# Performance work log

Hardware: AMD Instinct MI355X
Metric: run time of the kernel (lower is better)

Reference implementation:

```python
import jax, jax.numpy as jnp
import numpy as np

N_HEAD = 16
D_MODEL = 1024
D_HEAD = D_MODEL // N_HEAD
B, T = 2, 2048


def setup_inputs() -> dict:
    key = jax.random.key(0)
    k1, k2, k3 = jax.random.split(key, 3)
    x = jax.random.normal(k1, (B, T, D_MODEL), dtype=jnp.float32)
    w_attn = jax.random.normal(k2, (3 * D_MODEL, D_MODEL), dtype=jnp.float32) * (D_MODEL ** -0.5)
    w_proj = jax.random.normal(k3, (D_MODEL, D_MODEL), dtype=jnp.float32) * (D_MODEL ** -0.5)
    return {"x": x, "w_attn": w_attn, "w_proj": w_proj}


def _rms_norm(x):
    eps = jnp.asarray(jnp.finfo(x.dtype).eps, x.dtype)
    var = jnp.mean(jnp.square(x), axis=-1, keepdims=True)
    return x * jax.lax.rsqrt(var + eps)


def _rotate_half(x):
    x1, x2 = jnp.split(x, 2, axis=-1)
    return jnp.concatenate((-x2, x1), axis=-1)


def reference(x, w_attn, w_proj):
    Bx, Tx, C = x.shape
    qkv = jnp.einsum('btc,fc->btf', x, w_attn)  # [B,T,3C]
    q, k, v = jnp.split(qkv, 3, axis=-1)
    # [B, H, T, Dh]
    q = q.reshape(Bx, Tx, N_HEAD, D_HEAD).transpose(0, 2, 1, 3)
    k = k.reshape(Bx, Tx, N_HEAD, D_HEAD).transpose(0, 2, 1, 3)
    v = v.reshape(Bx, Tx, N_HEAD, D_HEAD).transpose(0, 2, 1, 3)
    # QK RMSNorm (no learned weight)
    q = _rms_norm(q)
    k = _rms_norm(k)
    # Rotary embedding over full d_head: freqs tiled twice
    inv_freq = 1.0 / (10000.0 ** (jnp.arange(0, D_HEAD, 2, dtype=jnp.float32) / D_HEAD))
    t = jnp.arange(Tx, dtype=jnp.float32)
    freqs = jnp.einsum('i,j->ij', t, inv_freq)  # [T, Dh/2]
    emb = jnp.concatenate((freqs, freqs), axis=-1)  # [T, Dh]
    cos = jnp.cos(emb)[None, None, :, :]
    sin = jnp.sin(emb)[None, None, :, :]
    q = q * cos + _rotate_half(q) * sin
    k = k * cos + _rotate_half(k) * sin
    # Causal SDPA
    scale = D_HEAD ** -0.5
    scores = jnp.einsum('bhqd,bhkd->bhqk', q, k) * scale
    causal = jnp.tril(jnp.ones((Tx, Tx), dtype=bool))
    scores = jnp.where(causal[None, None], scores, jnp.asarray(-jnp.inf, scores.dtype))
    attn = jax.nn.softmax(scores, axis=-1)
    y = jnp.einsum('bhqk,bhkd->bhqd', attn, v)
    y = y.transpose(0, 2, 1, 3).reshape(Bx, Tx, C)
    return jnp.einsum('btc,oc->bto', y, w_proj)
```

## Files before the change

kernel.cpp:

```cpp
#include <hip/hip_runtime.h>
#include <cstdint>
#include <cstddef>


typedef short bf16x8 __attribute__((ext_vector_type(8)));
typedef float floatx4 __attribute__((ext_vector_type(4)));
typedef float floatx2 __attribute__((ext_vector_type(2)));
typedef unsigned short ushortx8 __attribute__((ext_vector_type(8)));
typedef unsigned short ushortx4 __attribute__((ext_vector_type(4)));
typedef unsigned int uintx2 __attribute__((ext_vector_type(2)));

#define DEVI __device__ __forceinline__

DEVI float bf2f(unsigned short u) {
    unsigned int x = ((unsigned int)u) << 16;
    return __builtin_bit_cast(float, x);
}
DEVI unsigned short f2bf(float f) {
    unsigned int u = __builtin_bit_cast(unsigned int, f);
    u += 0x7fffu + ((u >> 16) & 1u);
    return (unsigned short)(u >> 16);
}
DEVI unsigned int pkbf2(float a, float b) {
    unsigned int ua = __builtin_bit_cast(unsigned int, a) + 0x8000u;
    unsigned int ub = __builtin_bit_cast(unsigned int, b) + 0x8000u;
    return __builtin_amdgcn_perm(ub, ua, 0x07060302);
}

DEVI void glds16(const unsigned short* g, unsigned short* l) {
    __builtin_amdgcn_global_load_lds(
        (const __attribute__((address_space(1))) unsigned int*)g,
        (__attribute__((address_space(3))) unsigned int*)l, 16, 0, 0);
}

DEVI void cast8(unsigned short* dst, const float* src) {
    floatx4 a = *(const floatx4*)src;
    floatx4 b = *(const floatx4*)(src + 4);
    ushortx8 o;
    o[0] = f2bf(a[0]); o[1] = f2bf(a[1]); o[2] = f2bf(a[2]); o[3] = f2bf(a[3]);
    o[4] = f2bf(b[0]); o[5] = f2bf(b[1]); o[6] = f2bf(b[2]); o[7] = f2bf(b[3]);
    *(ushortx8*)dst = o;
}

__global__ __launch_bounds__(256)
void cast_inputs(const float* __restrict__ x, const float* __restrict__ wa,
                 const float* __restrict__ wp,
                 unsigned short* __restrict__ xb, unsigned short* __restrict__ wab,
                 unsigned short* __restrict__ wpb, float* __restrict__ ropetab)
{
    size_t g = (size_t)blockIdx.x * 256 + threadIdx.x;
    size_t stride = (size_t)gridDim.x * 256;
    for (size_t i = g; i < (4194304 / 8); i += stride) cast8(xb  + i * 8, x  + i * 8);
    for (size_t i = g; i < (3145728 / 8); i += stride) cast8(wab + i * 8, wa + i * 8);
    for (size_t i = g; i < (1048576 / 8); i += stride) cast8(wpb + i * 8, wp + i * 8);
    for (size_t i = g; i < 65536; i += stride) {
        int t = (int)(i >> 5), f = (int)(i & 31);
        float ang = (float)t * __expf(-(float)f * 0.28782313662425572f);
        float sn, cs;
        __sincosf(ang, &sn, &cs);
        ropetab[2 * i]     = cs;
        ropetab[2 * i + 1] = sn;
    }
}

__global__ __launch_bounds__(512, 2)
void gemm_qkv_8ph(const unsigned short* __restrict__ A,
                  const unsigned short* __restrict__ B,
                  const float* __restrict__ ropetab,
                  unsigned short* __restrict__ Cqk,
                  unsigned short* __restrict__ Vt)
{
    __shared__ __align__(16) unsigned short lds[2][2][256 * 64];

    const int tid  = threadIdx.x;
    const int lane = tid & 63;
    const int w    = tid >> 6;
    const int wm   = w >> 2;
    const int wn   = w & 3;
    const int quad = lane >> 4;
    const int lm   = lane & 15;

    const int lin = blockIdx.y * 12 + blockIdx.x;
    const int s   = (lin & 7) * 24 + (lin >> 3);
    const int m0  = (s / 12) * 256;
    const int n0  = (s % 12) * 256;

    const int srow = tid >> 3;
    const int scol = (((tid & 7) ^ ((tid >> 3) & 7)) * 8);
    const int ldst = w * 512;

#define STG_A(u, WBi, kq) glds16(&A[(size_t)(m0 + (u) * 64 + srow) * 1024 + (kq) + scol], \
                                 &lds[WBi][0][(u) * 4096 + ldst])
#define STG_B(u, WBi, kq) glds16(&B[(size_t)(n0 + (u) * 64 + srow) * 1024 + (kq) + scol], \
                                 &lds[WBi][1][(u) * 4096 + ldst])
#define RD_A(RBi, rrow, kk) (*(const bf16x8*)&lds[RBi][0][(rrow) * 64 + ((((kk) * 4 + quad) ^ ((rrow) & 7)) * 8)])
#define RD_B(RBi, rrow, kk) (*(const bf16x8*)&lds[RBi][1][(rrow) * 64 + ((((kk) * 4 + quad) ^ ((rrow) & 7)) * 8)])

    floatx4 acc[8][4] = {};
    bf16x8 afr[4][2];
    bf16x8 bfr[4][2];

#define MQ(MB, JB)                                                              \
  do {                                                                          \
    _Pragma("unroll")                                                           \
    for (int kk = 0; kk < 2; ++kk)                                              \
      _Pragma("unroll")                                                         \
      for (int mi = 0; mi < 4; ++mi)                                            \
        _Pragma("unroll")                                                       \
        for (int j2 = 0; j2 < 2; ++j2)                                          \
          acc[(MB) + mi][(JB) + j2] = __builtin_amdgcn_mfma_f32_16x16x32_bf16(  \
              afr[mi][kk], bfr[(JB) + j2][kk], acc[(MB) + mi][(JB) + j2], 0, 0, 0); \
  } while (0)

#define TILE(RBi, WBi, KT, LASTF)                                               \
  do {                                                                          \
    const int kn = ((KT) + 1) * 64;                                             \
                \
    if (!(LASTF)) { STG_B(0, WBi, kn); STG_B(1, WBi, kn); }                     \
    _Pragma("unroll")                                                           \
    for (int kk = 0; kk < 2; ++kk) {                                            \
      _Pragma("unroll")                                                         \
      for (int mi = 0; mi < 4; ++mi)                                            \
        afr[mi][kk] = RD_A(RBi, wm * 128 + mi * 16 + lm, kk);                   \
      _Pragma("unroll")                                                         \
      for (int j2 = 0; j2 < 2; ++j2)                                            \
        bfr[j2][kk] = RD_B(RBi, wn * 64 + j2 * 16 + lm, kk);                    \
    }                                                                           \
    asm volatile("s_waitcnt lgkmcnt(8)" ::: "memory");                          \
    __builtin_amdgcn_s_barrier();                                               \
    asm volatile("s_waitcnt lgkmcnt(0)" ::: "memory");                          \
    __builtin_amdgcn_s_setprio(1); MQ(0, 0); __builtin_amdgcn_s_setprio(0);     \
    __builtin_amdgcn_s_barrier();                                               \
               \
    if (!(LASTF)) { STG_B(2, WBi, kn); STG_B(3, WBi, kn); }                     \
    _Pragma("unroll")                                                           \
    for (int kk = 0; kk < 2; ++kk)                                              \
      _Pragma("unroll")                                                         \
      for (int j2 = 0; j2 < 2; ++j2)                                            \
        bfr[2 + j2][kk] = RD_B(RBi, wn * 64 + (2 + j2) * 16 + lm, kk);          \
    if (!(LASTF)) { asm volatile("s_waitcnt vmcnt(4)" ::: "memory"); }          \
    else          { asm volatile("s_waitcnt vmcnt(0)" ::: "memory"); }          \
    __builtin_amdgcn_s_barrier();                                               \
    asm volatile("s_waitcnt lgkmcnt(0)" ::: "memory");                          \
    __builtin_amdgcn_s_setprio(1); MQ(0, 2); __builtin_amdgcn_s_setprio(0);     \
    __builtin_amdgcn_s_barrier();                                               \
                           \
    if (!(LASTF)) { STG_A(0, WBi, kn); STG_A(2, WBi, kn); }                     \
    _Pragma("unroll")                                                           \
    for (int kk = 0; kk < 2; ++kk)                                              \
      _Pragma("unroll")                                                         \
      for (int mi = 0; mi < 4; ++mi)                                            \
        afr[mi][kk] = RD_A(RBi, wm * 128 + 64 + mi * 16 + lm, kk);              \
    __builtin_amdgcn_s_barrier();                                               \
    asm volatile("s_waitcnt lgkmcnt(0)" ::: "memory");                          \
    __builtin_amdgcn_s_setprio(1); MQ(4, 2); __builtin_amdgcn_s_setprio(0);     \
    __builtin_amdgcn_s_barrier();                                               \
      \
    if (!(LASTF)) { STG_A(1, WBi, kn); STG_A(3, WBi, kn);                       \
                    asm volatile("s_waitcnt vmcnt(2)" ::: "memory"); }          \
    __builtin_amdgcn_s_barrier();                                               \
    __builtin_amdgcn_s_setprio(1); MQ(4, 0); __builtin_amdgcn_s_setprio(0);     \
    __builtin_amdgcn_s_barrier();                                               \
  } while (0)

    STG_B(0, 0, 0); STG_B(1, 0, 0); STG_B(2, 0, 0); STG_B(3, 0, 0);
    STG_A(0, 0, 0); STG_A(2, 0, 0); STG_A(1, 0, 0); STG_A(3, 0, 0);
    asm volatile("s_waitcnt vmcnt(2)" ::: "memory");
    __builtin_amdgcn_s_barrier();

    for (int kt = 0; kt < 14; kt += 2) {
        TILE(0, 1, kt, false);
        TILE(1, 0, kt + 1, false);
    }
    TILE(0, 1, 14, false);
    TILE(1, 0, 15, true);

    const bool is_v = (n0 + wn * 64) >= 2048;
    if (!is_v) {
        const floatx2* rtab = (const floatx2*)ropetab;
        #pragma unroll
        for (int mi = 0; mi < 8; ++mi) {
            float rn[4];
            #pragma unroll
            for (int r = 0; r < 4; ++r) {
                float ss = 0.0f;
                #pragma unroll
                for (int j = 0; j < 4; ++j) ss += acc[mi][j][r] * acc[mi][j][r];
                ss += __shfl_xor(ss, 1, 64);
                ss += __shfl_xor(ss, 2, 64);
                ss += __shfl_xor(ss, 4, 64);
                ss += __shfl_xor(ss, 8, 64);
                rn[r] = rsqrtf(ss * (1.0f / 64.0f) + 1.1920929e-07f);
            }
            #pragma unroll
            for (int r = 0; r < 4; ++r) {
                int row = m0 + wm * 128 + mi * 16 + quad * 4 + r;
                int t = row & 2047;
                floatx2 cs0 = rtab[t * 32 + lm];
                floatx2 cs1 = rtab[t * 32 + 16 + lm];
                float g = rn[r];
                #pragma unroll
                for (int j = 0; j < 4; ++j) {
                    int d = j * 16 + lm;
                    float cs = (j & 1) ? cs1[0] : cs0[0];
                    float sn = (j & 1) ? cs1[1] : cs0[1];
                    float v  = acc[mi][j][r] * g;
                    float vp = acc[mi][j ^ 2][r] * g;
                    float sgn = (d < 32) ? -1.0f : 1.0f;
                    Cqk[(size_t)row * 2048 + (n0 + wn * 64 + d)] =
                        f2bf(v * cs + sgn * vp * sn);
                }
            }
        }
    } else {
        #pragma unroll
        for (int mi = 0; mi < 8; ++mi)
            #pragma unroll
            for (int j = 0; j < 4; ++j) {
                int col  = n0 + wn * 64 + j * 16 + lm;
                int row0 = m0 + wm * 128 + mi * 16 + quad * 4;
                int bq = row0 >> 11, t0 = row0 & 2047;
                ushortx4 pk;
                #pragma unroll
                for (int r = 0; r < 4; ++r) pk[r] = f2bf(acc[mi][j][r]);
                *(ushortx4*)&Vt[((size_t)(bq * 1024 + (col - 2048))) * 2048 + t0] = pk;
            }
    }
#undef TILE
#undef MQ
#undef RD_A
#undef RD_B
#undef STG_A
#undef STG_B
}

template <bool QKV_SPLIT, int BN, int BK>
__global__ __launch_bounds__(256)
void gemm_bt(const unsigned short* __restrict__ A, const unsigned short* __restrict__ B,
             unsigned short* __restrict__ Cqk, float* __restrict__ Cf,
             unsigned short* __restrict__ Vt, int M, int N, int K)
{
    constexpr int WCOLS = (BN == 128) ? 2 : 1;
    constexpr int WROWS = 4 / WCOLS;
    constexpr int MI    = 128 / (16 * WROWS);
    constexpr int LPR   = BK / 8;
    constexpr int RPI   = 64 / LPR;

    __shared__ __align__(16) unsigned short As[128 * BK];
    __shared__ __align__(16) unsigned short Bs[BN * BK];

    const int tid  = threadIdx.x;
    const int lane = tid & 63;
    const int w    = tid >> 6;
    const int wm   = w / WCOLS, wn = w % WCOLS;
    const int quad = lane >> 4;
    const int lm   = lane & 15;
    const int m0 = blockIdx.y * 128;
    const int n0 = blockIdx.x * BN;
    const int sr = lane / LPR;
    const int sc = (lane % LPR) * 8;

    floatx4 acc[MI][4] = {};

    for (int k0 = 0; k0 < K; k0 += BK) {
        __syncthreads();
        #pragma unroll
        for (int i = 0; i < 32 / RPI; ++i) {
            int r = w * 32 + i * RPI;
            glds16(&A[(size_t)(m0 + r + sr) * K + k0 + sc], &As[r * BK]);
        }
        #pragma unroll
        for (int i = 0; i < (BN / 4) / RPI; ++i) {
            int r = w * (BN / 4) + i * RPI;
            glds16(&B[(size_t)(n0 + r + sr) * K + k0 + sc], &Bs[r * BK]);
        }
        __syncthreads();

        #pragma unroll
        for (int kk = 0; kk < BK / 32; ++kk) {
            bf16x8 a[MI];
            #pragma unroll
            for (int i = 0; i < MI; ++i)
                a[i] = *(const bf16x8*)&As[(wm * (16 * MI) + i * 16 + lm) * BK + kk * 32 + quad * 8];
            #pragma unroll
            for (int j = 0; j < 4; ++j) {
                bf16x8 b = *(const bf16x8*)&Bs[(wn * 64 + j * 16 + lm) * BK + kk * 32 + quad * 8];
                #pragma unroll
                for (int i = 0; i < MI; ++i)
                    acc[i][j] = __builtin_amdgcn_mfma_f32_16x16x32_bf16(a[i], b, acc[i][j], 0, 0, 0);
            }
        }
    }

    if constexpr (QKV_SPLIT) {
    } else {
        #pragma unroll
        for (int i = 0; i < MI; ++i)
            #pragma unroll
            for (int j = 0; j < 4; ++j) {
                int col  = n0 + wn * 64 + j * 16 + lm;
                int row0 = m0 + wm * (16 * MI) + i * 16 + quad * 4;
                #pragma unroll
                for (int r = 0; r < 4; ++r)
                    Cf[(size_t)(row0 + r) * N + col] = acc[i][j][r];
            }
    }
}

#define ATTN_STEP(KSc, VSc, KSn, VSn, KT, DG, LAST)                            \
  do {                                                                         \
    if (!(LAST)) {                                                             \
      *(ushortx8*)&(KSn)[r0 * LD + pc] = kreg0;                                \
      *(ushortx8*)&(KSn)[r1 * LD + pc] = kreg1;                                \
      *(ushortx8*)&(VSn)[r0 * LD + pc] = vreg0;                                \
      *(ushortx8*)&(VSn)[r1 * LD + pc] = vreg1;                                \
      if ((KT) + 2 <= qt) {                                                    \
        kreg0 = *(const ushortx8*)kp0; kreg1 = *(const ushortx8*)kp1;          \
        vreg0 = *(const ushortx8*)vp0; vreg1 = *(const ushortx8*)vp1;          \
        kp0 += (size_t)64 * 2048; kp1 += (size_t)64 * 2048;                    \
        vp0 += 64; vp1 += 64;                                                  \
      }                                                                        \
    }                                                                          \
    floatx4 sa[4] = {};                                                        \
    _Pragma("unroll")                                                          \
    for (int kk = 0; kk < 2; ++kk)                                             \
      _Pragma("unroll")                                                        \
      for (int j = 0; j < 4; ++j) {                                            \
        bf16x8 kf = *(const bf16x8*)&(KSc)[(j * 16 + lm) * LD + kk * 32 + quad * 8]; \
        sa[j] = __builtin_amdgcn_mfma_f32_16x16x32_bf16(kf, qf[kk], sa[j], 0, 0, 0); \
      }                                                                        \
    _Pragma("unroll")                                                          \
    for (int j = 0; j < 4; ++j) {                                              \
      float p0 = exp2f(sa[j][0] * c1 - c2);                                    \
      float p1 = exp2f(sa[j][1] * c1 - c2);                                    \
      float p2 = exp2f(sa[j][2] * c1 - c2);                                    \
      float p3 = exp2f(sa[j][3] * c1 - c2);                                    \
      if (DG) {                                                                \
        int kb = (KT) * 64 + j * 16 + quad * 4;                                \
        if (kb + 0 > qrow) p0 = 0.0f;                                          \
        if (kb + 1 > qrow) p1 = 0.0f;                                          \
        if (kb + 2 > qrow) p2 = 0.0f;                                          \
        if (kb + 3 > qrow) p3 = 0.0f;                                          \
      }                                                                        \
      uintx2 pk;                                                               \
      pk[0] = pkbf2(p0, p1);                                                   \
      pk[1] = pkbf2(p2, p3);                                                   \
      *(uintx2*)&QPs[(w * 16 + lm) * LD + j * 16 + quad * 4] = pk;             \
    }                                                                          \
    _Pragma("unroll")                                                          \
    for (int kk = 0; kk < 2; ++kk) {                                           \
      bf16x8 pf = *(const bf16x8*)&QPs[(w * 16 + lm) * LD + kk * 32 + quad * 8]; \
      _Pragma("unroll")                                                        \
      for (int j = 0; j < 4; ++j) {                                            \
        bf16x8 vf = *(const bf16x8*)&(VSc)[(j * 16 + lm) * LD + kk * 32 + quad * 8]; \
        o[j] = __builtin_amdgcn_mfma_f32_16x16x32_bf16(pf, vf, o[j], 0, 0, 0); \
      }                                                                        \
      l_acc = __builtin_amdgcn_mfma_f32_16x16x32_bf16(pf, ones, l_acc, 0, 0, 0); \
    }                                                                          \
    if (!(LAST)) __syncthreads();                                              \
  } while (0)

__global__ __launch_bounds__(256)
void attention(const unsigned short* __restrict__ qk,
               const unsigned short* __restrict__ Vt,
               unsigned short* __restrict__ Y)
{
    constexpr int LD = 72;
    __shared__ __align__(16) unsigned short QPs[64 * LD];
    __shared__ __align__(16) unsigned short Ks0[64 * LD];
    __shared__ __align__(16) unsigned short Ks1[64 * LD];
    __shared__ __align__(16) unsigned short Vs0[64 * LD];
    __shared__ __align__(16) unsigned short Vs1[64 * LD];

    const int tid  = threadIdx.x;
    const int lane = tid & 63;
    const int w    = tid >> 6;
    const int quad = lane >> 4;
    const int lm   = lane & 15;

    const int bh = blockIdx.x;
    const int qt = 31 - blockIdx.y;
    const int b  = bh >> 4, h = bh & 15;
    const int q0 = qt * 64;
    const int qrow = q0 + w * 16 + lm;

    const int r0 = tid >> 3, r1 = r0 + 32, pc = (tid & 7) * 8;
    const unsigned short* kp0 = qk + (size_t)b * 2048 * 2048 + 1024 + h * 64
                              + (size_t)r0 * 2048 + pc;
    const unsigned short* kp1 = kp0 + (size_t)32 * 2048;
    const unsigned short* vp0 = Vt + (size_t)bh * 64 * 2048 + (size_t)r0 * 2048 + pc;
    const unsigned short* vp1 = vp0 + (size_t)32 * 2048;

    #pragma unroll
    for (int i = 0; i < 2; ++i) {
        int c = i * 256 + tid, row = c >> 3, col = (c & 7) * 8;
        *(ushortx8*)&QPs[row * LD + col] =
            *(const ushortx8*)&qk[((size_t)(b * 2048 + q0 + row)) * 2048 + h * 64 + col];
    }

    ushortx8 kreg0 = *(const ushortx8*)kp0, kreg1 = *(const ushortx8*)kp1;
    ushortx8 vreg0 = *(const ushortx8*)vp0, vreg1 = *(const ushortx8*)vp1;
    kp0 += (size_t)64 * 2048; kp1 += (size_t)64 * 2048;
    vp0 += 64; vp1 += 64;
    *(ushortx8*)&Ks0[r0 * LD + pc] = kreg0;
    *(ushortx8*)&Ks0[r1 * LD + pc] = kreg1;
    *(ushortx8*)&Vs0[r0 * LD + pc] = vreg0;
    *(ushortx8*)&Vs0[r1 * LD + pc] = vreg1;
    if (qt >= 1) {
        kreg0 = *(const ushortx8*)kp0; kreg1 = *(const ushortx8*)kp1;
        vreg0 = *(const ushortx8*)vp0; vreg1 = *(const ushortx8*)vp1;
        kp0 += (size_t)64 * 2048; kp1 += (size_t)64 * 2048;
        vp0 += 64; vp1 += 64;
    }
    __syncthreads();

    bf16x8 qf[2];
    #pragma unroll
    for (int kk = 0; kk < 2; ++kk)
        qf[kk] = *(const bf16x8*)&QPs[(w * 16 + lm) * LD + kk * 32 + quad * 8];

    bf16x8 ones;
    #pragma unroll
    for (int i = 0; i < 8; ++i) ones[i] = (short)0x3F80;

    floatx4 o[4] = {};
    floatx4 l_acc = {};
    const float c1 = 0.125f * 1.44269504f;
    const float c2 = 8.0f   * 1.44269504f;

    int kt = 0;
    for (; kt + 1 < qt; kt += 2) {
        ATTN_STEP(Ks0, Vs0, Ks1, Vs1, kt,     false, false);
        ATTN_STEP(Ks1, Vs1, Ks0, Vs0, kt + 1, false, false);
    }
    if (kt < qt) {
        ATTN_STEP(Ks0, Vs0, Ks1, Vs1, kt, false, false);
        ATTN_STEP(Ks1, Vs1, Ks0, Vs0, qt, true, true);
    } else {
        ATTN_STEP(Ks0, Vs0, Ks1, Vs1, qt, true, true);
    }

    float rinv[4];
    #pragma unroll
    for (int r = 0; r < 4; ++r) rinv[r] = 1.0f / l_acc[r];

    #pragma unroll
    for (int j = 0; j < 4; ++j) {
        int colg = h * 64 + j * 16 + lm;
        #pragma unroll
        for (int r = 0; r < 4; ++r) {
            int rowg = q0 + w * 16 + quad * 4 + r;
            Y[((size_t)(b * 2048 + rowg)) * 1024 + colg] = f2bf(o[j][r] * rinv[r]);
        }
    }
}

extern "C" void kernel_launch(void* const* d_in, const int* in_sizes, int n_in,
                              void* d_out, int out_size, void* d_ws, size_t ws_size,
                              hipStream_t stream)
{
    const float* x      = (const float*)d_in[0];
    const float* w_attn = (const float*)d_in[1];
    const float* w_proj = (const float*)d_in[2];
    float* out = (float*)d_out;

    unsigned short* qkbuf = (unsigned short*)d_ws;
    unsigned short* Vtb   = qkbuf + (size_t)4096 * 2048;
    unsigned short* y     = Vtb   + (size_t)32 * 64 * 2048;
    unsigned short* wpb   = y     + (size_t)4096 * 1024;
    unsigned short* xb  = (unsigned short*)d_out;
    unsigned short* wab = xb + (size_t)4096 * 1024;
    float* ropetab = (float*)(wab + (size_t)3072 * 1024);

    dim3 blk(256);
    cast_inputs<<<dim3(1024), blk, 0, stream>>>(x, w_attn, w_proj, xb, wab, wpb, ropetab);
    gemm_qkv_8ph<<<dim3(12, 16), dim3(512), 0, stream>>>(xb, wab, ropetab, qkbuf, Vtb);
    attention<<<dim3(32, 32), blk, 0, stream>>>(qkbuf, Vtb, y);
    gemm_bt<false, 64, 64>
        <<<dim3(16, 32), blk, 0, stream>>>(y, wpb, nullptr, out, nullptr, 4096, 1024, 1024);
}
```

Measured before the change: 176.2 us.

## Use 128-row query tiles with 512-thread attention blocks sharing K/V tiles

The attention kernel now processes 128 query rows per block with 8 waves (512 threads) instead of 64 rows with 4 waves. Each K/V tile loaded into shared memory is reused by twice as many query rows, which halves global K/V traffic and the number of blocks. Each thread now stages one 16-byte chunk of K and V instead of two. The last two key tiles are treated as diagonal, with causal masking, to cover the 128-row block. The gemm_bt template also drops an unused QKV-split path, which is cleanup. The trade-off is more wasted masked work on diagonal tiles, fewer blocks for load balance, and larger shared-memory use per block.

New measurement: 178.7 us. No clear change (+1.4%).

```diff
diff --git a/kernel.cpp b/kernel.cpp
--- a/kernel.cpp
+++ b/kernel.cpp
@@ -115,7 +115,6 @@
 #define TILE(RBi, WBi, KT, LASTF)                                               \
   do {                                                                          \
     const int kn = ((KT) + 1) * 64;                                             \
-                \
     if (!(LASTF)) { STG_B(0, WBi, kn); STG_B(1, WBi, kn); }                     \
     _Pragma("unroll")                                                           \
     for (int kk = 0; kk < 2; ++kk) {                                            \
@@ -131,7 +130,6 @@
     asm volatile("s_waitcnt lgkmcnt(0)" ::: "memory");                          \
     __builtin_amdgcn_s_setprio(1); MQ(0, 0); __builtin_amdgcn_s_setprio(0);     \
     __builtin_amdgcn_s_barrier();                                               \
-               \
     if (!(LASTF)) { STG_B(2, WBi, kn); STG_B(3, WBi, kn); }                     \
     _Pragma("unroll")                                                           \
     for (int kk = 0; kk < 2; ++kk)                                              \
@@ -144,7 +142,6 @@
     asm volatile("s_waitcnt lgkmcnt(0)" ::: "memory");                          \
     __builtin_amdgcn_s_setprio(1); MQ(0, 2); __builtin_amdgcn_s_setprio(0);     \
     __builtin_amdgcn_s_barrier();                                               \
-                           \
     if (!(LASTF)) { STG_A(0, WBi, kn); STG_A(2, WBi, kn); }                     \
     _Pragma("unroll")                                                           \
     for (int kk = 0; kk < 2; ++kk)                                              \
@@ -155,7 +152,6 @@
     asm volatile("s_waitcnt lgkmcnt(0)" ::: "memory");                          \
     __builtin_amdgcn_s_setprio(1); MQ(4, 2); __builtin_amdgcn_s_setprio(0);     \
     __builtin_amdgcn_s_barrier();                                               \
-      \
     if (!(LASTF)) { STG_A(1, WBi, kn); STG_A(3, WBi, kn);                       \
                     asm volatile("s_waitcnt vmcnt(2)" ::: "memory"); }          \
     __builtin_amdgcn_s_barrier();                                               \
@@ -234,11 +230,10 @@
 #undef STG_B
 }
 
-template <bool QKV_SPLIT, int BN, int BK>
+template <int BN, int BK>
 __global__ __launch_bounds__(256)
 void gemm_bt(const unsigned short* __restrict__ A, const unsigned short* __restrict__ B,
-             unsigned short* __restrict__ Cqk, float* __restrict__ Cf,
-             unsigned short* __restrict__ Vt, int M, int N, int K)
+             float* __restrict__ Cf, int M, int N, int K)
 {
     constexpr int WCOLS = (BN == 128) ? 2 : 1;
     constexpr int WROWS = 4 / WCOLS;
@@ -292,33 +287,26 @@
         }
     }
 
-    if constexpr (QKV_SPLIT) {
-    } else {
-        #pragma unroll
-        for (int i = 0; i < MI; ++i)
-            #pragma unroll
-            for (int j = 0; j < 4; ++j) {
-                int col  = n0 + wn * 64 + j * 16 + lm;
-                int row0 = m0 + wm * (16 * MI) + i * 16 + quad * 4;
-                #pragma unroll
-                for (int r = 0; r < 4; ++r)
-                    Cf[(size_t)(row0 + r) * N + col] = acc[i][j][r];
-            }
-    }
+    #pragma unroll
+    for (int i = 0; i < MI; ++i)
+        #pragma unroll
+        for (int j = 0; j < 4; ++j) {
+            int col  = n0 + wn * 64 + j * 16 + lm;
+            int row0 = m0 + wm * (16 * MI) + i * 16 + quad * 4;
+            #pragma unroll
+            for (int r = 0; r < 4; ++r)
+                Cf[(size_t)(row0 + r) * N + col] = acc[i][j][r];
+        }
 }
 
 #define ATTN_STEP(KSc, VSc, KSn, VSn, KT, DG, LAST)                            \
   do {                                                                         \
     if (!(LAST)) {                                                             \
-      *(ushortx8*)&(KSn)[r0 * LD + pc] = kreg0;                                \
-      *(ushortx8*)&(KSn)[r1 * LD + pc] = kreg1;                                \
-      *(ushortx8*)&(VSn)[r0 * LD + pc] = vreg0;                                \
-      *(ushortx8*)&(VSn)[r1 * LD + pc] = vreg1;                                \
-      if ((KT) + 2 <= qt) {                                                    \
-        kreg0 = *(const ushortx8*)kp0; kreg1 = *(const ushortx8*)kp1;          \
-        vreg0 = *(const ushortx8*)vp0; vreg1 = *(const ushortx8*)vp1;          \
-        kp0 += (size_t)64 * 2048; kp1 += (size_t)64 * 2048;                    \
-        vp0 += 64; vp1 += 64;                                                  \
+      *(ushortx8*)&(KSn)[r0 * LD + pc] = kreg;                                 \
+      *(ushortx8*)&(VSn)[r0 * LD + pc] = vreg;                                 \
+      if ((KT) + 2 <= lastk) {                                                 \
+        kreg = *(const ushortx8*)kp0; vreg = *(const ushortx8*)vp0;            \
+        kp0 += (size_t)64 * 2048; vp0 += 64;                                   \
       }                                                                        \
     }                                                                          \
     floatx4 sa[4] = {};                                                        \
@@ -360,13 +348,13 @@
     if (!(LAST)) __syncthreads();                                              \
   } while (0)
 
-__global__ __launch_bounds__(256)
+__global__ __launch_bounds__(512)
 void attention(const unsigned short* __restrict__ qk,
                const unsigned short* __restrict__ Vt,
                unsigned short* __restrict__ Y)
 {
     constexpr int LD = 72;
-    __shared__ __align__(16) unsigned short QPs[64 * LD];
+    __shared__ __align__(16) unsigned short QPs[128 * LD];
     __shared__ __align__(16) unsigned short Ks0[64 * LD];
     __shared__ __align__(16) unsigned short Ks1[64 * LD];
     __shared__ __align__(16) unsigned short Vs0[64 * LD];
@@ -379,38 +367,32 @@
     const int lm   = lane & 15;
 
     const int bh = blockIdx.x;
-    const int qt = 31 - blockIdx.y;
+    const int qt = 15 - blockIdx.y;
     const int b  = bh >> 4, h = bh & 15;
-    const int q0 = qt * 64;
+    const int q0 = qt * 128;
     const int qrow = q0 + w * 16 + lm;
-
-    const int r0 = tid >> 3, r1 = r0 + 32, pc = (tid & 7) * 8;
+    const int lastk = 2 * qt + 1;
+
+    const int r0 = tid >> 3, pc = (tid & 7) * 8;
     const unsigned short* kp0 = qk + (size_t)b * 2048 * 2048 + 1024 + h * 64
                               + (size_t)r0 * 2048 + pc;
-    const unsigned short* kp1 = kp0 + (size_t)32 * 2048;
     const unsigned short* vp0 = Vt + (size_t)bh * 64 * 2048 + (size_t)r0 * 2048 + pc;
-    const unsigned short* vp1 = vp0 + (size_t)32 * 2048;
 
     #pragma unroll
     for (int i = 0; i < 2; ++i) {
-        int c = i * 256 + tid, row = c >> 3, col = (c & 7) * 8;
+        int c = i * 512 + tid, row = c >> 3, col = (c & 7) * 8;
         *(ushortx8*)&QPs[row * LD + col] =
             *(const ushortx8*)&qk[((size_t)(b * 2048 + q0 + row)) * 2048 + h * 64 + col];
     }
 
-    ushortx8 kreg0 = *(const ushortx8*)kp0, kreg1 = *(const ushortx8*)kp1;
-    ushortx8 vreg0 = *(const ushortx8*)vp0, vreg1 = *(const ushortx8*)vp1;
-    kp0 += (size_t)64 * 2048; kp1 += (size_t)64 * 2048;
-    vp0 += 64; vp1 += 64;
-    *(ushortx8*)&Ks0[r0 * LD + pc] = kreg0;
-    *(ushortx8*)&Ks0[r1 * LD + pc] = kreg1;
-    *(ushortx8*)&Vs0[r0 * LD + pc] = vreg0;
-    *(ushortx8*)&Vs0[r1 * LD + pc] = vreg1;
-    if (qt >= 1) {
-        kreg0 = *(const ushortx8*)kp0; kreg1 = *(const ushortx8*)kp1;
-        vreg0 = *(const ushortx8*)vp0; vreg1 = *(const ushortx8*)vp1;
-        kp0 += (size_t)64 * 2048; kp1 += (size_t)64 * 2048;
-        vp0 += 64; vp1 += 64;
+    ushortx8 kreg = *(const ushortx8*)kp0;
+    ushortx8 vreg = *(const ushortx8*)vp0;
+    kp0 += (size_t)64 * 2048; vp0 += 64;
+    *(ushortx8*)&Ks0[r0 * LD + pc] = kreg;
+    *(ushortx8*)&Vs0[r0 * LD + pc] = vreg;
+    if (lastk >= 1) {
+        kreg = *(const ushortx8*)kp0; vreg = *(const ushortx8*)vp0;
+        kp0 += (size_t)64 * 2048; vp0 += 64;
     }
     __syncthreads();
 
@@ -429,16 +411,12 @@
     const float c2 = 8.0f   * 1.44269504f;
 
     int kt = 0;
-    for (; kt + 1 < qt; kt += 2) {
+    for (; kt + 3 < 2 * qt + 2; kt += 2) {
         ATTN_STEP(Ks0, Vs0, Ks1, Vs1, kt,     false, false);
         ATTN_STEP(Ks1, Vs1, Ks0, Vs0, kt + 1, false, false);
     }
-    if (kt < qt) {
-        ATTN_STEP(Ks0, Vs0, Ks1, Vs1, kt, false, false);
-        ATTN_STEP(Ks1, Vs1, Ks0, Vs0, qt, true, true);
-    } else {
-        ATTN_STEP(Ks0, Vs0, Ks1, Vs1, qt, true, true);
-    }
+    ATTN_STEP(Ks0, Vs0, Ks1, Vs1, kt,     true, false);
+    ATTN_STEP(Ks1, Vs1, Ks0, Vs0, kt + 1, true, true);
 
     float rinv[4];
     #pragma unroll
@@ -475,7 +453,7 @@
     dim3 blk(256);
     cast_inputs<<<dim3(1024), blk, 0, stream>>>(x, w_attn, w_proj, xb, wab, wpb, ropetab);
     gemm_qkv_8ph<<<dim3(12, 16), dim3(512), 0, stream>>>(xb, wab, ropetab, qkbuf, Vtb);
-    attention<<<dim3(32, 32), blk, 0, stream>>>(qkbuf, Vtb, y);
-    gemm_bt<false, 64, 64>
-        <<<dim3(16, 32), blk, 0, stream>>>(y, wpb, nullptr, out, nullptr, 4096, 1024, 1024);
-}
+    attention<<<dim3(32, 16), dim3(512), 0, stream>>>(qkbuf, Vtb, y);
+    gemm_bt<64, 64>
+        <<<dim3(16, 32), blk, 0, stream>>>(y, wpb, out, 4096, 1024, 1024);
+}
```
